# Kernel optimization log

Hardware: AMD Instinct MI355X
Metric: run time of the kernel (lower is better)

The kernel has to match this reference:

```python
import jax, jax.numpy as jnp
import numpy as np

H = 8        # heads
W = 64       # window size
SHIFT = True
DIM = 512
SCALE = (DIM // H) ** -0.5


def setup_inputs() -> dict:
    key = jax.random.key(0)
    k1, k2, k3, k4 = jax.random.split(key, 4)
    x = jax.random.normal(k1, (8, 4096, DIM), dtype=jnp.float32)
    w_qkv = jax.random.normal(k2, (3 * DIM, DIM), dtype=jnp.float32) * 0.02
    w_proj = jax.random.normal(k3, (DIM, DIM), dtype=jnp.float32) * 0.02
    b_proj = jax.random.normal(k4, (DIM,), dtype=jnp.float32) * 0.02
    return {"x": x, "w_qkv": w_qkv, "w_proj": w_proj, "b_proj": b_proj}


def reference(x, w_qkv, w_proj, b_proj):
    B, N, C = x.shape
    if SHIFT:
        x = jnp.roll(x, -W // 2, axis=1)
    pad = (W - N % W) % W  # static Python int
    if pad:
        x = jnp.pad(x, ((0, 0), (0, pad), (0, 0)))
    nw = x.shape[1] // W
    xw = x.reshape(B * nw, W, C)                     # (B', W, C)
    qkv = xw @ w_qkv.T                               # (B', W, 3C)
    qkv = qkv.reshape(B * nw, W, 3, H, C // H)
    q, k, v = qkv[:, :, 0], qkv[:, :, 1], qkv[:, :, 2]  # (B', W, H, dh)
    # NOTE: faithful to source -- heads are NOT moved before matmul, so
    # attention is over the head axis: attn shape (B', W, H, H).
    attn = jnp.einsum('bwhd,bwgd->bwhg', q, k) * SCALE
    attn = jax.nn.softmax(attn, axis=-1)
    out = jnp.einsum('bwhg,bwgd->bwhd', attn, v)     # (B', W, H, dh)
    # transpose(1,2) then raw reshape, exactly as torch does (channel scramble)
    out = out.transpose(0, 2, 1, 3).reshape(B * nw, W, C)
    out = out @ w_proj.T + b_proj
    out = out.reshape(B, nw * W, C)[:, :N]
    if SHIFT:
        out = jnp.roll(out, W // 2, axis=1)
    return out
```

## Files before the change

kernel.cpp:

```cpp
#include <hip/hip_runtime.h>
#include <math.h>

typedef __attribute__((ext_vector_type(8))) short short8;
typedef __attribute__((ext_vector_type(4))) float float4v;

#define KDIM  512
#define NQKV  1536

__device__ __forceinline__ unsigned short f2bf(float f) {
    unsigned int u = __float_as_uint(f);
    u += 0x7FFFu + ((u >> 16) & 1u);
    return (unsigned short)(u >> 16);
}
__device__ __forceinline__ float bf2f(unsigned short u) {
    return __uint_as_float(((unsigned int)u) << 16);
}

__device__ __forceinline__ void gl2lds16(const unsigned short* g, unsigned short* l) {
    __builtin_amdgcn_global_load_lds(
        (const __attribute__((address_space(1))) void*)g,
        (__attribute__((address_space(3))) void*)l, 16, 0, 0);
}

__global__ __launch_bounds__(256) void cast_all_kernel(const float* __restrict__ x,
                                                       const float* __restrict__ wqkv,
                                                       const float* __restrict__ wproj,
                                                       unsigned short* __restrict__ xb,
                                                       unsigned short* __restrict__ wqkvb,
                                                       unsigned short* __restrict__ wprojb) {
    if (blockIdx.x < 16384) {
        int tid = blockIdx.x * 256 + threadIdx.x;
        int t = tid >> 7;
        int c = (tid & 127) << 2;
        int b = t >> 12, n = t & 4095;
        int src = (b << 12) | ((n + 32) & 4095);
        float4 v = *(const float4*)(x + (((size_t)src) << 9) + c);
        ushort4 o;
        o.x = f2bf(v.x); o.y = f2bf(v.y); o.z = f2bf(v.z); o.w = f2bf(v.w);
        *(ushort4*)(xb + (((size_t)t) << 9) + c) = o;
    } else {
        int tid = (blockIdx.x - 16384) * 256 + threadIdx.x;
        int e = tid << 2;
        if (e < NQKV * KDIM) {
            float4 v = *(const float4*)(wqkv + e);
            ushort4 o; o.x = f2bf(v.x); o.y = f2bf(v.y); o.z = f2bf(v.z); o.w = f2bf(v.w);
            *(ushort4*)(wqkvb + e) = o;
        } else {
            int e2 = e - NQKV * KDIM;
            float4 v = *(const float4*)(wproj + e2);
            ushort4 o; o.x = f2bf(v.x); o.y = f2bf(v.y); o.z = f2bf(v.z); o.w = f2bf(v.w);
            *(ushort4*)(wprojb + e2) = o;
        }
    }
}

template<int N, bool PROJ>
__global__ __launch_bounds__(256, 2) void gemm_kernel(
        const unsigned short* __restrict__ A,
        const unsigned short* __restrict__ B,
        unsigned short* __restrict__ Cb,
        float* __restrict__ Cf,
        const float* __restrict__ bias) {
    __shared__ __align__(16) unsigned short As[128 * 64];
    __shared__ __align__(16) unsigned short Bs[128 * 64];
    constexpr int GX  = N / 128;
    constexpr int PER = (GX * 256) / 8;
    const int wgid = blockIdx.y * GX + blockIdx.x;
    const int swz  = (wgid & 7) * PER + (wgid >> 3);
    const int bm = swz / GX;
    const int bn = swz % GX;

    const int tid = threadIdx.x;
    const int wave = tid >> 6, lane = tid & 63;
    const int quad = lane >> 4, l16 = lane & 15;
    const int wm = (wave >> 1) * 64, wn = (wave & 1) * 64;
    const int srow = lane >> 3;
    const int scol = ((lane & 7) ^ srow) * 8;

    float4v acc[4][4] = {};

    const unsigned short* Abase = A + (size_t)(bm * 128) * KDIM;
    const unsigned short* Bbase = B + (size_t)(bn * 128) * KDIM;

    for (int k0 = 0; k0 < KDIM; k0 += 64) {
        #pragma unroll
        for (int j = 0; j < 4; j++) {
            int chunk = j * 4 + wave;
            int row = chunk * 8 + srow;
            gl2lds16(Abase + (size_t)row * KDIM + k0 + scol, As + chunk * 512);
            gl2lds16(Bbase + (size_t)row * KDIM + k0 + scol, Bs + chunk * 512);
        }
        __syncthreads();
        #pragma unroll
        for (int ki = 0; ki < 2; ki++) {
            short8 af[4], bf[4];
            #pragma unroll
            for (int mi = 0; mi < 4; mi++) {
                int r = wm + mi * 16 + l16;
                int blk = (ki * 4 + quad) ^ (l16 & 7);
                af[mi] = *(const short8*)(As + r * 64 + blk * 8);
            }
            #pragma unroll
            for (int ni = 0; ni < 4; ni++) {
                int r = wn + ni * 16 + l16;
                int blk = (ki * 4 + quad) ^ (l16 & 7);
                bf[ni] = *(const short8*)(Bs + r * 64 + blk * 8);
            }
            #pragma unroll
            for (int mi = 0; mi < 4; mi++)
                #pragma unroll
                for (int ni = 0; ni < 4; ni++)
                    acc[mi][ni] = __builtin_amdgcn_mfma_f32_16x16x32_bf16(
                        af[mi], bf[ni], acc[mi][ni], 0, 0, 0);
        }
        __syncthreads();
    }

    #pragma unroll
    for (int mi = 0; mi < 4; mi++) {
        #pragma unroll
        for (int r = 0; r < 4; r++) {
            int m = bm * 128 + wm + mi * 16 + quad * 4 + r;
            if (!PROJ) {
                #pragma unroll
                for (int ni = 0; ni < 4; ni++) {
                    int n = bn * 128 + wn + ni * 16 + l16;
                    Cb[(size_t)m * N + n] = f2bf(acc[mi][ni][r]);
                }
            } else {
                int b = m >> 12, p = m & 4095;
                int nrow = (p + 32) & 4095;
                float* orow = Cf + (((size_t)((b << 12) | nrow)) << 9);
                #pragma unroll
                for (int ni = 0; ni < 4; ni++) {
                    int n = bn * 128 + wn + ni * 16 + l16;
                    orow[n] = acc[mi][ni][r] + bias[n];
                }
            }
        }
    }
}

__global__ __launch_bounds__(256) void attn_kernel(const unsigned short* __restrict__ qkvb,
                                                   unsigned short* __restrict__ aob) {
    const int tid = blockIdx.x * 256 + threadIdx.x;
    const int t = tid >> 3, h = tid & 7;
    const unsigned short* base = qkvb + (size_t)t * NQKV;

    float s[8];
    {
        short8 qs[8];
        #pragma unroll
        for (int dc = 0; dc < 8; dc++)
            qs[dc] = *(const short8*)(base + h * 64 + dc * 8);
        float qv[64];
        #pragma unroll
        for (int dc = 0; dc < 8; dc++)
            #pragma unroll
            for (int j = 0; j < 8; j++)
                qv[dc * 8 + j] = bf2f((unsigned short)qs[dc][j]);
        #pragma unroll
        for (int g = 0; g < 8; g++) {
            const unsigned short* krow = base + 512 + g * 64;
            float acc = 0.f;
            #pragma unroll
            for (int dc = 0; dc < 8; dc++) {
                short8 ks = *(const short8*)(krow + dc * 8);
                #pragma unroll
                for (int j = 0; j < 8; j++)
                    acc += qv[dc * 8 + j] * bf2f((unsigned short)ks[j]);
            }
            s[g] = acc;
        }
    }

    float mx = s[0];
    #pragma unroll
    for (int g = 1; g < 8; g++) mx = fmaxf(mx, s[g]);
    float p[8], sum = 0.f;
    #pragma unroll
    for (int g = 0; g < 8; g++) { p[g] = __expf((s[g] - mx) * 0.125f); sum += p[g]; }
    float inv = 1.f / sum;
    #pragma unroll
    for (int g = 0; g < 8; g++) p[g] *= inv;

    float o[64];
    #pragma unroll
    for (int j = 0; j < 64; j++) o[j] = 0.f;
    #pragma unroll
    for (int g = 0; g < 8; g++) {
        const unsigned short* vrow = base + 1024 + g * 64;
        #pragma unroll
        for (int dc = 0; dc < 8; dc++) {
            short8 vs = *(const short8*)(vrow + dc * 8);
            #pragma unroll
            for (int j = 0; j < 8; j++)
                o[dc * 8 + j] += p[g] * bf2f((unsigned short)vs[j]);
        }
    }

    int win = t >> 6, w = t & 63;
    unsigned short* dst = aob + (size_t)(win * 64 + h * 8 + (w >> 3)) * 512 + (w & 7) * 64;
    #pragma unroll
    for (int dc = 0; dc < 16; dc++) {
        ushort4 ov;
        ov.x = f2bf(o[dc * 4 + 0]); ov.y = f2bf(o[dc * 4 + 1]);
        ov.z = f2bf(o[dc * 4 + 2]); ov.w = f2bf(o[dc * 4 + 3]);
        *(ushort4*)(dst + dc * 4) = ov;
    }
}

extern "C" void kernel_launch(void* const* d_in, const int* in_sizes, int n_in,
                              void* d_out, int out_size, void* d_ws, size_t ws_size,
                              hipStream_t stream) {
    const float* x      = (const float*)d_in[0];
    const float* w_qkv  = (const float*)d_in[1];
    const float* w_proj = (const float*)d_in[2];
    const float* b_proj = (const float*)d_in[3];
    float* out = (float*)d_out;

    char* ws = (char*)d_ws;
    unsigned short* xb     = (unsigned short*)(ws);
    unsigned short* wqkvb  = (unsigned short*)(ws + 33554432);
    unsigned short* wprojb = (unsigned short*)(ws + 35127296);
    unsigned short* qkvb   = (unsigned short*)(ws + 35651584);
    unsigned short* aob    = (unsigned short*)(ws + 136314880);

    cast_all_kernel<<<17408, 256, 0, stream>>>(x, w_qkv, w_proj, xb, wqkvb, wprojb);
    gemm_kernel<NQKV, false><<<dim3(12, 256), 256, 0, stream>>>(xb, wqkvb, qkvb, nullptr, nullptr);
    attn_kernel<<<1024, 256, 0, stream>>>(qkvb, aob);
    gemm_kernel<512, true><<<dim3(4, 256), 256, 0, stream>>>(aob, wprojb, nullptr, out, b_proj);
}
```

Before: 247.5 us.

## Fuse head-axis attention with output projection into one per-window kernel

Merges the attention kernel and the projection GEMM into one kernel that handles one 64-token window per block. The scrambled attention output is written to swizzled LDS instead of a global buffer, then multiplied by the projection weights with MFMA, and the bias and the roll-back shift are applied in the epilogue. This removes the global write and reread of the intermediate (about 32 MB of bf16) and one launch. In exchange, projection weights are read straight from global memory without LDS staging, each block holds 64 KB of LDS, and the grid drops to 512 blocks, which may lower occupancy.

Result: no change. 248.1 us (+0.2%).

```diff
diff --git a/kernel.cpp b/kernel.cpp
--- a/kernel.cpp
+++ b/kernel.cpp
@@ -54,13 +54,11 @@
     }
 }
 
-template<int N, bool PROJ>
+template<int N>
 __global__ __launch_bounds__(256, 2) void gemm_kernel(
         const unsigned short* __restrict__ A,
         const unsigned short* __restrict__ B,
-        unsigned short* __restrict__ Cb,
-        float* __restrict__ Cf,
-        const float* __restrict__ bias) {
+        unsigned short* __restrict__ Cb) {
     __shared__ __align__(16) unsigned short As[128 * 64];
     __shared__ __align__(16) unsigned short Bs[128 * 64];
     constexpr int GX  = N / 128;
@@ -121,92 +119,136 @@
         #pragma unroll
         for (int r = 0; r < 4; r++) {
             int m = bm * 128 + wm + mi * 16 + quad * 4 + r;
-            if (!PROJ) {
-                #pragma unroll
-                for (int ni = 0; ni < 4; ni++) {
-                    int n = bn * 128 + wn + ni * 16 + l16;
-                    Cb[(size_t)m * N + n] = f2bf(acc[mi][ni][r]);
+            #pragma unroll
+            for (int ni = 0; ni < 4; ni++) {
+                int n = bn * 128 + wn + ni * 16 + l16;
+                Cb[(size_t)m * N + n] = f2bf(acc[mi][ni][r]);
+            }
+        }
+    }
+}
+
+__global__ __launch_bounds__(512, 2) void attnproj_kernel(
+        const unsigned short* __restrict__ qkvb,
+        const unsigned short* __restrict__ wprojb,
+        const float* __restrict__ bias,
+        float* __restrict__ out) {
+    __shared__ __align__(16) unsigned short Asf[64 * 512];
+    const int tid = threadIdx.x;
+    const int win = blockIdx.x;
+
+    {
+        const int w = tid >> 3, h = tid & 7;
+        const int t = win * 64 + w;
+        const unsigned short* base = qkvb + (size_t)t * NQKV;
+
+        float s[8];
+        {
+            short8 qs[8];
+            #pragma unroll
+            for (int dc = 0; dc < 8; dc++)
+                qs[dc] = *(const short8*)(base + h * 64 + dc * 8);
+            float qv[64];
+            #pragma unroll
+            for (int dc = 0; dc < 8; dc++)
+                #pragma unroll
+                for (int j = 0; j < 8; j++)
+                    qv[dc * 8 + j] = bf2f((unsigned short)qs[dc][j]);
+            #pragma unroll
+            for (int g = 0; g < 8; g++) {
+                const unsigned short* krow = base + 512 + g * 64;
+                float acc = 0.f;
+                #pragma unroll
+                for (int dc = 0; dc < 8; dc++) {
+                    short8 ks = *(const short8*)(krow + dc * 8);
+                    #pragma unroll
+                    for (int j = 0; j < 8; j++)
+                        acc += qv[dc * 8 + j] * bf2f((unsigned short)ks[j]);
                 }
-            } else {
-                int b = m >> 12, p = m & 4095;
-                int nrow = (p + 32) & 4095;
-                float* orow = Cf + (((size_t)((b << 12) | nrow)) << 9);
-                #pragma unroll
-                for (int ni = 0; ni < 4; ni++) {
-                    int n = bn * 128 + wn + ni * 16 + l16;
-                    orow[n] = acc[mi][ni][r] + bias[n];
-                }
-            }
-        }
-    }
-}
-
-__global__ __launch_bounds__(256) void attn_kernel(const unsigned short* __restrict__ qkvb,
-                                                   unsigned short* __restrict__ aob) {
-    const int tid = blockIdx.x * 256 + threadIdx.x;
-    const int t = tid >> 3, h = tid & 7;
-    const unsigned short* base = qkvb + (size_t)t * NQKV;
-
-    float s[8];
-    {
-        short8 qs[8];
-        #pragma unroll
-        for (int dc = 0; dc < 8; dc++)
-            qs[dc] = *(const short8*)(base + h * 64 + dc * 8);
-        float qv[64];
-        #pragma unroll
-        for (int dc = 0; dc < 8; dc++)
-            #pragma unroll
-            for (int j = 0; j < 8; j++)
-                qv[dc * 8 + j] = bf2f((unsigned short)qs[dc][j]);
+                s[g] = acc;
+            }
+        }
+
+        float mx = s[0];
+        #pragma unroll
+        for (int g = 1; g < 8; g++) mx = fmaxf(mx, s[g]);
+        float p[8], sum = 0.f;
+        #pragma unroll
+        for (int g = 0; g < 8; g++) { p[g] = __expf((s[g] - mx) * 0.125f); sum += p[g]; }
+        float inv = 1.f / sum;
+        #pragma unroll
+        for (int g = 0; g < 8; g++) p[g] *= inv;
+
+        float o[64];
+        #pragma unroll
+        for (int j = 0; j < 64; j++) o[j] = 0.f;
         #pragma unroll
         for (int g = 0; g < 8; g++) {
-            const unsigned short* krow = base + 512 + g * 64;
-            float acc = 0.f;
+            const unsigned short* vrow = base + 1024 + g * 64;
             #pragma unroll
             for (int dc = 0; dc < 8; dc++) {
-                short8 ks = *(const short8*)(krow + dc * 8);
+                short8 vs = *(const short8*)(vrow + dc * 8);
                 #pragma unroll
                 for (int j = 0; j < 8; j++)
-                    acc += qv[dc * 8 + j] * bf2f((unsigned short)ks[j]);
-            }
-            s[g] = acc;
-        }
-    }
-
-    float mx = s[0];
+                    o[dc * 8 + j] += p[g] * bf2f((unsigned short)vs[j]);
+            }
+        }
+
+        int lw = h * 8 + (w >> 3);
+        int keyr = (lw ^ (lw >> 3)) & 7;
+        unsigned short* dstrow = Asf + lw * 512;
+        #pragma unroll
+        for (int dc = 0; dc < 8; dc++) {
+            short8 pk;
+            #pragma unroll
+            for (int j = 0; j < 8; j++) pk[j] = (short)f2bf(o[dc * 8 + j]);
+            int cb = (w & 7) * 8 + dc;
+            *(short8*)(dstrow + ((cb ^ keyr) * 8)) = pk;
+        }
+    }
+    __syncthreads();
+
+    const int wave = tid >> 6, lane = tid & 63;
+    const int quad = lane >> 4, l16 = lane & 15;
+    const int wc = wave;
+
+    float4v acc[4][4] = {};
     #pragma unroll
-    for (int g = 1; g < 8; g++) mx = fmaxf(mx, s[g]);
-    float p[8], sum = 0.f;
+    for (int ks = 0; ks < 16; ks++) {
+        short8 af[4], bfr[4];
+        #pragma unroll
+        for (int mi = 0; mi < 4; mi++) {
+            int r = mi * 16 + l16;
+            int kb = ks * 4 + quad;
+            af[mi] = *(const short8*)(Asf + r * 512 + ((kb ^ ((r ^ (r >> 3)) & 7)) * 8));
+        }
+        #pragma unroll
+        for (int ni = 0; ni < 4; ni++) {
+            int r = wc * 64 + ni * 16 + l16;
+            bfr[ni] = *(const short8*)(wprojb + (size_t)r * KDIM + ks * 32 + quad * 8);
+        }
+        #pragma unroll
+        for (int mi = 0; mi < 4; mi++)
+            #pragma unroll
+            for (int ni = 0; ni < 4; ni++)
+                acc[mi][ni] = __builtin_amdgcn_mfma_f32_16x16x32_bf16(
+                    af[mi], bfr[ni], acc[mi][ni], 0, 0, 0);
+    }
+
     #pragma unroll
-    for (int g = 0; g < 8; g++) { p[g] = __expf((s[g] - mx) * 0.125f); sum += p[g]; }
-    float inv = 1.f / sum;
-    #pragma unroll
-    for (int g = 0; g < 8; g++) p[g] *= inv;
-
-    float o[64];
-    #pragma unroll
-    for (int j = 0; j < 64; j++) o[j] = 0.f;
-    #pragma unroll
-    for (int g = 0; g < 8; g++) {
-        const unsigned short* vrow = base + 1024 + g * 64;
-        #pragma unroll
-        for (int dc = 0; dc < 8; dc++) {
-            short8 vs = *(const short8*)(vrow + dc * 8);
-            #pragma unroll
-            for (int j = 0; j < 8; j++)
-                o[dc * 8 + j] += p[g] * bf2f((unsigned short)vs[j]);
-        }
-    }
-
-    int win = t >> 6, w = t & 63;
-    unsigned short* dst = aob + (size_t)(win * 64 + h * 8 + (w >> 3)) * 512 + (w & 7) * 64;
-    #pragma unroll
-    for (int dc = 0; dc < 16; dc++) {
-        ushort4 ov;
-        ov.x = f2bf(o[dc * 4 + 0]); ov.y = f2bf(o[dc * 4 + 1]);
-        ov.z = f2bf(o[dc * 4 + 2]); ov.w = f2bf(o[dc * 4 + 3]);
-        *(ushort4*)(dst + dc * 4) = ov;
+    for (int mi = 0; mi < 4; mi++) {
+        #pragma unroll
+        for (int r4 = 0; r4 < 4; r4++) {
+            int m = win * 64 + mi * 16 + quad * 4 + r4;
+            int b = m >> 12, pp = m & 4095;
+            int nrow = (pp + 32) & 4095;
+            float* orow = out + (((size_t)((b << 12) | nrow)) << 9);
+            #pragma unroll
+            for (int ni = 0; ni < 4; ni++) {
+                int n = wc * 64 + ni * 16 + l16;
+                orow[n] = acc[mi][ni][r4] + bias[n];
+            }
+        }
     }
 }
 
@@ -224,10 +266,8 @@
     unsigned short* wqkvb  = (unsigned short*)(ws + 33554432);
     unsigned short* wprojb = (unsigned short*)(ws + 35127296);
     unsigned short* qkvb   = (unsigned short*)(ws + 35651584);
-    unsigned short* aob    = (unsigned short*)(ws + 136314880);
 
     cast_all_kernel<<<17408, 256, 0, stream>>>(x, w_qkv, w_proj, xb, wqkvb, wprojb);
-    gemm_kernel<NQKV, false><<<dim3(12, 256), 256, 0, stream>>>(xb, wqkvb, qkvb, nullptr, nullptr);
-    attn_kernel<<<1024, 256, 0, stream>>>(qkvb, aob);
-    gemm_kernel<512, true><<<dim3(4, 256), 256, 0, stream>>>(aob, wprojb, nullptr, out, b_proj);
-}
+    gemm_kernel<NQKV><<<dim3(12, 256), 256, 0, stream>>>(xb, wqkvb, qkvb);
+    attnproj_kernel<<<512, 512, 0, stream>>>(qkvb, wprojb, b_proj, out);
+}
```
